# Kernel optimization log

Hardware: AMD Instinct MI355X
Metric: run time of the kernel (lower is better)

The kernel has to match this reference:

```python
import jax, jax.numpy as jnp
import numpy as np

N_NODES = 50000
N_EDGES = 800000


def sage_conv(x, src, dst, W_l, b_l, W_r, num_nodes):
    """PyG SAGEConv with mean aggregation: out = lin_l(mean_agg(neighbors)) + lin_r(x)."""
    # gather source-node features per edge, scatter-mean into destination nodes
    msg = x[src]                                                   # [E, F]
    agg = jax.ops.segment_sum(msg, dst, num_segments=num_nodes)    # [N, F]
    cnt = jax.ops.segment_sum(jnp.ones((src.shape[0],), x.dtype), dst,
                              num_segments=num_nodes)              # [N]
    agg = agg / jnp.maximum(cnt, 1.0)[:, None]
    return agg @ W_l + b_l + x @ W_r


def setup_inputs() -> dict:
    key = jax.random.key(0)
    ks = jax.random.split(key, 8)
    d_in, d_hid, d_out = 128, 256, 128
    s = lambda k, shape, fan: jax.random.normal(k, shape, jnp.float32) / np.sqrt(fan)
    return {
        "x": jax.random.normal(ks[0], (N_NODES, d_in), jnp.float32),
        "edge_index": jax.random.randint(ks[1], (2, N_EDGES), 0, N_NODES, jnp.int64),
        "W1_l": s(ks[2], (d_in, d_hid), d_in),
        "b1": jnp.zeros((d_hid,), jnp.float32),
        "W1_r": s(ks[3], (d_in, d_hid), d_in),
        "W2_l": s(ks[4], (d_hid, d_out), d_hid),
        "b2": jnp.zeros((d_out,), jnp.float32),
        "W2_r": s(ks[5], (d_hid, d_out), d_hid),
    }


def reference(x, edge_index, W1_l, b1, W1_r, W2_l, b2, W2_r):
    src, dst = edge_index[0], edge_index[1]
    n = x.shape[0]
    h = sage_conv(x, src, dst, W1_l, b1, W1_r, n)
    h = jax.nn.relu(h)  # dropout p=0.0 -> identity
    out = sage_conv(h, src, dst, W2_l, b2, W2_r, n)
    return out
```

## Files before the change

### kernel.cpp

```cpp
#include <hip/hip_runtime.h>
#include <hip/hip_bf16.h>
#include <stdint.h>

#define NN 50000
#define NE 800000
#define NB 196
#define EPB 2048
#define NBLK ((NE + EPB - 1) / EPB)
#define BCAP 8192

typedef __attribute__((ext_vector_type(8))) __bf16 bf16x8;
typedef __attribute__((ext_vector_type(4))) float f32x4;
typedef __attribute__((ext_vector_type(4))) int i32x4;

__device__ __forceinline__ float bflo(uint32_t u) { return __uint_as_float(u << 16); }
__device__ __forceinline__ float bfhi(uint32_t u) { return __uint_as_float(u & 0xffff0000u); }
__device__ __forceinline__ uint16_t f2bf(float f) {
    uint32_t u = __float_as_uint(f);
    u += 0x7fffu + ((u >> 16) & 1u);
    return (uint16_t)(u >> 16);
}
__device__ __forceinline__ float bf2f(uint16_t h) { return __uint_as_float(((uint32_t)h) << 16); }

__device__ __forceinline__ int xcd_swz(int bid, int nwg) {
    int q = nwg >> 3, r = nwg & 7;
    int xcd = bid & 7, idx = bid >> 3;
    int base = (xcd < r) ? xcd * (q + 1) : r * (q + 1) + (xcd - r) * q;
    return base + idx;
}

__device__ __forceinline__ int detect_i64(const int* ei, int* sh_cnt) {
    int t = threadIdx.x;
    if (t == 0) *sh_cnt = 0;
    __syncthreads();
    if (t < 64) atomicAdd(sh_cnt, (ei[2 * t + 1] != 0) ? 1 : 0);
    __syncthreads();
    return (*sh_cnt < 4) ? 1 : 0;
}

__device__ __forceinline__ int detect_fp32(const uint32_t* xu, int* sh_cnt) {
    int t = threadIdx.x;
    if (t == 0) *sh_cnt = 0;
    __syncthreads();
    uint32_t u = xu[t & 255];
    uint32_t lo = u & 0xffffu;
    uint32_t e = (lo >> 7) & 0xffu;
    int ok = (lo == 0u) || (e >= 96u && e <= 150u);
    if (t < 256) atomicAdd(sh_cnt, ok);
    __syncthreads();
    return (*sh_cnt < 192) ? 1 : 0;
}

__global__ __launch_bounds__(256) void scatter1(const int* __restrict__ ei,
                                                int* __restrict__ bucket_cur,
                                                uint32_t* __restrict__ staging) {
    __shared__ int hist[NB];
    __shared__ int curs[NB];
    __shared__ int shc;
    int fl = detect_i64(ei, &shc);
    int t = threadIdx.x;
    for (int i = t; i < NB; i += 256) hist[i] = 0;
    __syncthreads();
    int base = blockIdx.x * EPB;
    for (int i = 0; i < EPB; i += 256) {
        int e = base + i + t;
        if (e < NE) {
            int d = fl ? ei[2 * NE + 2 * e] : ei[NE + e];
            atomicAdd(&hist[d >> 8], 1);
        }
    }
    __syncthreads();
    for (int i = t; i < NB; i += 256)
        curs[i] = (hist[i] > 0) ? atomicAdd(&bucket_cur[i], hist[i]) : 0;
    __syncthreads();
    for (int i = 0; i < EPB; i += 256) {
        int e = base + i + t;
        if (e < NE) {
            int s, d;
            if (fl) { s = ei[2 * e]; d = ei[2 * NE + 2 * e]; }
            else    { s = ei[e];     d = ei[NE + e]; }
            int b = d >> 8;
            int p = atomicAdd(&curs[b], 1);
            staging[b * BCAP + p] = ((uint32_t)(d & 0xff) << 16) | (uint32_t)s;
        }
    }
}

#define NORMX_BLKS 6250
__global__ __launch_bounds__(256) void csr_norm(const uint32_t* __restrict__ staging,
                                                const int* __restrict__ bucket_cur,
                                                const void* __restrict__ x,
                                                const void* __restrict__ w1l, const void* __restrict__ b1,
                                                const void* __restrict__ w1r, const void* __restrict__ w2l,
                                                const void* __restrict__ b2, const void* __restrict__ w2r,
                                                int* __restrict__ row_start, int* __restrict__ deg,
                                                float* __restrict__ inv_deg, int* __restrict__ csr,
                                                uint32_t* __restrict__ xb,
                                                uint16_t* __restrict__ w1l_sw, uint16_t* __restrict__ w1r_sw,
                                                uint16_t* __restrict__ w2l_sw, uint16_t* __restrict__ w2r_sw,
                                                uint16_t* __restrict__ bias_buf) {
    int blk = blockIdx.x;
    int t = threadIdx.x;
    if (blk < NB) {
        __shared__ int degs[256];
        __shared__ int sm[256];
        __shared__ int curs[256];
        int beg = blk * BCAP, cnt = bucket_cur[blk];
        degs[t] = 0;
        __syncthreads();
        for (int i = t; i < cnt; i += 256) atomicAdd(&degs[(staging[beg + i] >> 16) & 0xff], 1);
        __syncthreads();
        int d = degs[t];
        sm[t] = d;
        __syncthreads();
        for (int o = 1; o < 256; o <<= 1) {
            int x2 = (t >= o) ? sm[t - o] : 0;
            __syncthreads();
            sm[t] += x2;
            __syncthreads();
        }
        int excl = sm[t] - d;
        curs[t] = excl;
        int node = blk * 256 + t;
        if (node < NN) {
            row_start[node] = beg + excl;
            deg[node] = d;
            inv_deg[node] = 1.0f / (float)(d > 0 ? d : 1);
        }
        __syncthreads();
        for (int i = t; i < cnt; i += 256) {
            uint32_t u = staging[beg + i];
            int dl = (u >> 16) & 0xff;
            int p = atomicAdd(&curs[dl], 1);
            csr[beg + p] = (int)(u & 0xffffu);
        }
        return;
    }
    __shared__ int shc;
    int fp32 = detect_fp32((const uint32_t*)x, &shc);
    int nb = blk - NB;
    if (nb < NORMX_BLKS) {
        int i = nb * 256 + t;
        if (fp32) {
            f32x4 v = ((const f32x4*)x)[i];
            uint2 o;
            o.x = (uint32_t)f2bf(v[0]) | ((uint32_t)f2bf(v[1]) << 16);
            o.y = (uint32_t)f2bf(v[2]) | ((uint32_t)f2bf(v[3]) << 16);
            ((uint2*)xb)[i] = o;
        } else {
            ((uint2*)xb)[i] = ((const uint2*)x)[i];
        }
        return;
    }
    int tid = (nb - NORMX_BLKS) * 256 + t;
    if (tid < 16384) {
        int frag = tid >> 6, lane = tid & 63;
        const void* srcw; uint16_t* dst; int N; int fl;
        if (frag < 64)       { srcw = w1l; dst = w1l_sw; N = 256; fl = frag; }
        else if (frag < 128) { srcw = w1r; dst = w1r_sw; N = 256; fl = frag - 64; }
        else if (frag < 192) { srcw = w2l; dst = w2l_sw; N = 128; fl = frag - 128; }
        else                 { srcw = w2r; dst = w2r_sw; N = 128; fl = frag - 192; }
        int NTm = N >> 4;
        int kt = fl / NTm, nt = fl - kt * NTm;
        int k0 = kt * 32 + (lane >> 4) * 8, n = nt * 16 + (lane & 15);
        uint16_t* d = dst + (size_t)fl * 512 + lane * 8;
#pragma unroll
        for (int j = 0; j < 8; j++) {
            int si = (k0 + j) * N + n;
            d[j] = fp32 ? f2bf(((const float*)srcw)[si]) : ((const uint16_t*)srcw)[si];
        }
    } else if (tid < 16384 + 384) {
        int j = tid - 16384;
        const void* s = (j < 256) ? b1 : b2;
        int jj = (j < 256) ? j : j - 256;
        bias_buf[j] = fp32 ? f2bf(((const float*)s)[jj]) : ((const uint16_t*)s)[jj];
    }
}

__global__ __launch_bounds__(256) void agg_mean_v2(const uint32_t* __restrict__ xu,
                                                   const int* __restrict__ row_start,
                                                   const int* __restrict__ deg,
                                                   const int* __restrict__ csr,
                                                   const float* __restrict__ inv_deg,
                                                   uint32_t* __restrict__ outu) {
    int wave = threadIdx.x >> 6, lane = threadIdx.x & 63;
    int half = lane >> 5, l = lane & 31;
    int node = blockIdx.x * 8 + wave * 2 + half;
    int beg = row_start[node], end = beg + deg[node];
    float lx[8], hx[8], ly[8], hy[8];
#pragma unroll
    for (int k = 0; k < 8; k++) { lx[k] = 0.f; hx[k] = 0.f; ly[k] = 0.f; hy[k] = 0.f; }
    int j = beg;
    for (; j + 8 <= end; j += 8) {
        int idx[8];
#pragma unroll
        for (int k = 0; k < 8; k++) idx[k] = csr[j + k];
#pragma unroll
        for (int k = 0; k < 8; k++) {
            uint2 v = *(const uint2*)(xu + (size_t)idx[k] * 64 + l * 2);
            lx[k] += bflo(v.x); hx[k] += bfhi(v.x);
            ly[k] += bflo(v.y); hy[k] += bfhi(v.y);
        }
    }
    for (; j < end; j++) {
        uint2 v = *(const uint2*)(xu + (size_t)csr[j] * 64 + l * 2);
        lx[0] += bflo(v.x); hx[0] += bfhi(v.x);
        ly[0] += bflo(v.y); hy[0] += bfhi(v.y);
    }
    float sc = inv_deg[node];
    float r0 = (((lx[0] + lx[1]) + (lx[2] + lx[3])) + ((lx[4] + lx[5]) + (lx[6] + lx[7]))) * sc;
    float r1 = (((hx[0] + hx[1]) + (hx[2] + hx[3])) + ((hx[4] + hx[5]) + (hx[6] + hx[7]))) * sc;
    float r2 = (((ly[0] + ly[1]) + (ly[2] + ly[3])) + ((ly[4] + ly[5]) + (ly[6] + ly[7]))) * sc;
    float r3 = (((hy[0] + hy[1]) + (hy[2] + hy[3])) + ((hy[4] + hy[5]) + (hy[6] + hy[7]))) * sc;
    uint2 o;
    o.x = (uint32_t)f2bf(r0) | ((uint32_t)f2bf(r1) << 16);
    o.y = (uint32_t)f2bf(r2) | ((uint32_t)f2bf(r3) << 16);
    *(uint2*)(outu + (size_t)node * 64 + l * 2) = o;
}

__global__ __launch_bounds__(256) void agg_final_v2(const uint32_t* __restrict__ tu,
                                                    const int* __restrict__ row_start,
                                                    const int* __restrict__ deg,
                                                    const int* __restrict__ csr,
                                                    const float* __restrict__ inv_deg,
                                                    const f32x4* __restrict__ u,
                                                    f32x4* __restrict__ out) {
    int wave = threadIdx.x >> 6, lane = threadIdx.x & 63;
    int half = lane >> 5, l = lane & 31;
    int node = blockIdx.x * 8 + wave * 2 + half;
    int beg = row_start[node], end = beg + deg[node];
    float lx[8], hx[8], ly[8], hy[8];
#pragma unroll
    for (int k = 0; k < 8; k++) { lx[k] = 0.f; hx[k] = 0.f; ly[k] = 0.f; hy[k] = 0.f; }
    int j = beg;
    for (; j + 8 <= end; j += 8) {
        int idx[8];
#pragma unroll
        for (int k = 0; k < 8; k++) idx[k] = csr[j + k];
#pragma unroll
        for (int k = 0; k < 8; k++) {
            uint2 v = *(const uint2*)(tu + (size_t)idx[k] * 64 + l * 2);
            lx[k] += bflo(v.x); hx[k] += bfhi(v.x);
            ly[k] += bflo(v.y); hy[k] += bfhi(v.y);
        }
    }
    for (; j < end; j++) {
        uint2 v = *(const uint2*)(tu + (size_t)csr[j] * 64 + l * 2);
        lx[0] += bflo(v.x); hx[0] += bfhi(v.x);
        ly[0] += bflo(v.y); hy[0] += bfhi(v.y);
    }
    float sc = inv_deg[node];
    f32x4 uv = u[(size_t)node * 32 + l];
    f32x4 r;
    r[0] = (((lx[0] + lx[1]) + (lx[2] + lx[3])) + ((lx[4] + lx[5]) + (lx[6] + lx[7]))) * sc + uv[0];
    r[1] = (((hx[0] + hx[1]) + (hx[2] + hx[3])) + ((hx[4] + hx[5]) + (hx[6] + hx[7]))) * sc + uv[1];
    r[2] = (((ly[0] + ly[1]) + (ly[2] + ly[3])) + ((ly[4] + ly[5]) + (ly[6] + ly[7]))) * sc + uv[2];
    r[3] = (((hy[0] + hy[1]) + (hy[2] + hy[3])) + ((hy[4] + hy[5]) + (hy[6] + hy[7]))) * sc + uv[3];
    out[(size_t)node * 32 + l] = r;
}

#define HW 264
__global__ __launch_bounds__(512) void fused_mlp(const uint16_t* __restrict__ AGG,
                                                 const uint16_t* __restrict__ XB,
                                                 const uint16_t* __restrict__ W1Lsw,
                                                 const uint16_t* __restrict__ W1Rsw,
                                                 const uint16_t* __restrict__ W2Lsw,
                                                 const uint16_t* __restrict__ W2Rsw,
                                                 const uint16_t* __restrict__ bias,
                                                 uint16_t* __restrict__ T,
                                                 float* __restrict__ U) {
    __shared__ __align__(16) uint16_t hbuf[64 * HW];
    int wg = xcd_swz(blockIdx.x, 782);
    int node0 = wg * 64;
    int tid = threadIdx.x;
    int wave = tid >> 6, lane = tid & 63;
    int wr = wave >> 2, wc = wave & 3;
    int m = lane & 15, q = lane >> 4;

    int ar[2];
#pragma unroll
    for (int rf = 0; rf < 2; rf++) {
        int r = node0 + wr * 32 + rf * 16 + m;
        ar[rf] = (r < NN) ? r : (NN - 1);
    }

    {
        f32x4 acc[2][4];
#pragma unroll
        for (int rf = 0; rf < 2; rf++)
#pragma unroll
            for (int nt = 0; nt < 4; nt++)
#pragma unroll
                for (int i = 0; i < 4; i++) acc[rf][nt][i] = 0.f;

#pragma unroll
        for (int kt = 0; kt < 4; kt++) {
            bf16x8 a10 = *(const bf16x8*)(AGG + (size_t)ar[0] * 128 + kt * 32 + q * 8);
            bf16x8 a11 = *(const bf16x8*)(AGG + (size_t)ar[1] * 128 + kt * 32 + q * 8);
            bf16x8 a20 = *(const bf16x8*)(XB + (size_t)ar[0] * 128 + kt * 32 + q * 8);
            bf16x8 a21 = *(const bf16x8*)(XB + (size_t)ar[1] * 128 + kt * 32 + q * 8);
#pragma unroll
            for (int nt = 0; nt < 4; nt++) {
                int gnt = wc * 4 + nt;
                bf16x8 B1 = *(const bf16x8*)(W1Lsw + ((size_t)(kt * 16 + gnt)) * 512 + lane * 8);
                bf16x8 B2 = *(const bf16x8*)(W1Rsw + ((size_t)(kt * 16 + gnt)) * 512 + lane * 8);
                acc[0][nt] = __builtin_amdgcn_mfma_f32_16x16x32_bf16(a10, B1, acc[0][nt], 0, 0, 0);
                acc[1][nt] = __builtin_amdgcn_mfma_f32_16x16x32_bf16(a11, B1, acc[1][nt], 0, 0, 0);
                acc[0][nt] = __builtin_amdgcn_mfma_f32_16x16x32_bf16(a20, B2, acc[0][nt], 0, 0, 0);
                acc[1][nt] = __builtin_amdgcn_mfma_f32_16x16x32_bf16(a21, B2, acc[1][nt], 0, 0, 0);
            }
        }
#pragma unroll
        for (int rf = 0; rf < 2; rf++)
#pragma unroll
            for (int nt = 0; nt < 4; nt++) {
                int cl = wc * 64 + nt * 16 + m;
                float bv = bf2f(bias[cl]);
#pragma unroll
                for (int i = 0; i < 4; i++) {
                    float v = fmaxf(acc[rf][nt][i] + bv, 0.f);
                    hbuf[(wr * 32 + rf * 16 + q * 4 + i) * HW + cl] = f2bf(v);
                }
            }
    }
    __syncthreads();

    f32x4 acc1[2][2], acc2[2][2];
#pragma unroll
    for (int rf = 0; rf < 2; rf++)
#pragma unroll
        for (int nt = 0; nt < 2; nt++)
#pragma unroll
            for (int i = 0; i < 4; i++) { acc1[rf][nt][i] = 0.f; acc2[rf][nt][i] = 0.f; }

#pragma unroll
    for (int kt = 0; kt < 8; kt++) {
        bf16x8 a0 = *(const bf16x8*)&hbuf[(wr * 32 + m) * HW + kt * 32 + q * 8];
        bf16x8 a1 = *(const bf16x8*)&hbuf[(wr * 32 + 16 + m) * HW + kt * 32 + q * 8];
#pragma unroll
        for (int nt = 0; nt < 2; nt++) {
            int gnt = wc * 2 + nt;
            bf16x8 BL = *(const bf16x8*)(W2Lsw + ((size_t)(kt * 8 + gnt)) * 512 + lane * 8);
            bf16x8 BR = *(const bf16x8*)(W2Rsw + ((size_t)(kt * 8 + gnt)) * 512 + lane * 8);
            acc1[0][nt] = __builtin_amdgcn_mfma_f32_16x16x32_bf16(a0, BL, acc1[0][nt], 0, 0, 0);
            acc1[1][nt] = __builtin_amdgcn_mfma_f32_16x16x32_bf16(a1, BL, acc1[1][nt], 0, 0, 0);
            acc2[0][nt] = __builtin_amdgcn_mfma_f32_16x16x32_bf16(a0, BR, acc2[0][nt], 0, 0, 0);
            acc2[1][nt] = __builtin_amdgcn_mfma_f32_16x16x32_bf16(a1, BR, acc2[1][nt], 0, 0, 0);
        }
    }
    __syncthreads();

    {
        uint16_t* st = hbuf;
#pragma unroll
        for (int rf = 0; rf < 2; rf++)
#pragma unroll
            for (int nt = 0; nt < 2; nt++) {
                int cl = wc * 32 + nt * 16 + m;
#pragma unroll
                for (int i = 0; i < 4; i++)
                    st[(wr * 32 + rf * 16 + q * 4 + i) * 136 + cl] = f2bf(acc1[rf][nt][i]);
            }
        __syncthreads();
#pragma unroll
        for (int rr = 0; rr < 2; rr++) {
            int row = rr * 32 + (tid >> 4);
            int grow = node0 + row;
            if (grow < NN)
                *(i32x4*)(T + (size_t)grow * 128 + (tid & 15) * 8) =
                    *(const i32x4*)&st[row * 136 + (tid & 15) * 8];
        }
        __syncthreads();
    }

    {
        float* su = (float*)hbuf;
#pragma unroll
        for (int rf = 0; rf < 2; rf++)
#pragma unroll
            for (int nt = 0; nt < 2; nt++) {
                int cl = wc * 32 + nt * 16 + m;
                float bv = bf2f(bias[256 + cl]);
#pragma unroll
                for (int i = 0; i < 4; i++)
                    su[(wr * 32 + rf * 16 + q * 4 + i) * 132 + cl] = acc2[rf][nt][i] + bv;
            }
        __syncthreads();
#pragma unroll
        for (int rr = 0; rr < 4; rr++) {
            int row = rr * 16 + (tid >> 5);
            int grow = node0 + row;
            if (grow < NN)
                *(f32x4*)(U + (size_t)grow * 128 + (tid & 31) * 4) =
                    *(const f32x4*)&su[row * 132 + (tid & 31) * 4];
        }
    }
}

extern "C" void kernel_launch(void* const* d_in, const int* in_sizes, int n_in,
                              void* d_out, int out_size, void* d_ws, size_t ws_size,
                              hipStream_t stream) {
    const void* x_raw  = d_in[0];
    const int*  ei     = (const int*)d_in[1];
    const void* W1l    = d_in[2];
    const void* b1     = d_in[3];
    const void* W1r    = d_in[4];
    const void* W2l    = d_in[5];
    const void* b2     = d_in[6];
    const void* W2r    = d_in[7];

    uint8_t* ws = (uint8_t*)d_ws;
    size_t off = 0;
    auto alloc = [&](size_t b) -> void* {
        void* p = ws + off;
        off += (b + 255) & ~(size_t)255;
        return p;
    };
    int*      bucket_cur  = (int*)alloc((NB + 4) * 4);
    int*      deg         = (int*)alloc((size_t)NN * 4);
    float*    inv_deg     = (float*)alloc((size_t)NN * 4);
    int*      row_start   = (int*)alloc((size_t)NN * 4);
    int*      csr         = (int*)alloc((size_t)NB * BCAP * 4);
    uint32_t* xb          = (uint32_t*)alloc((size_t)NN * 64 * 4);
    uint16_t* bias_buf    = (uint16_t*)alloc(384 * 2);
    uint16_t* agg         = (uint16_t*)alloc((size_t)NN * 128 * 2);
    uint16_t* t           = (uint16_t*)alloc((size_t)NN * 128 * 2);
    float*    u           = (float*)alloc((size_t)NN * 128 * 4);
    uint16_t* w1l_sw      = (uint16_t*)alloc(128 * 256 * 2);
    uint16_t* w1r_sw      = (uint16_t*)alloc(128 * 256 * 2);
    uint16_t* w2l_sw      = (uint16_t*)alloc(256 * 128 * 2);
    uint16_t* w2r_sw      = (uint16_t*)alloc(256 * 128 * 2);

    uint32_t* staging = (uint32_t*)t;

    hipMemsetAsync(bucket_cur, 0, NB * 4, stream);
    scatter1<<<NBLK, 256, 0, stream>>>(ei, bucket_cur, staging);
    csr_norm<<<NB + NORMX_BLKS + 66, 256, 0, stream>>>(staging, bucket_cur, x_raw,
                                                       W1l, b1, W1r, W2l, b2, W2r,
                                                       row_start, deg, inv_deg, csr,
                                                       xb, w1l_sw, w1r_sw, w2l_sw, w2r_sw, bias_buf);

    agg_mean_v2<<<NN / 8, 256, 0, stream>>>(xb, row_start, deg, csr, inv_deg, (uint32_t*)agg);
    fused_mlp<<<782, 512, 0, stream>>>(agg, (const uint16_t*)xb,
                                       w1l_sw, w1r_sw, w2l_sw, w2r_sw, bias_buf, t, u);
    agg_final_v2<<<NN / 8, 256, 0, stream>>>((const uint32_t*)t, row_start, deg, csr, inv_deg,
                                             (const f32x4*)u, (f32x4*)d_out);
}
```

Measured before the change: 238.1 us.

## Split final aggregation by column slice per XCD with atomic work queues

```diff
diff --git a/kernel.cpp b/kernel.cpp
--- a/kernel.cpp
+++ b/kernel.cpp
@@ -8,6 +8,7 @@
 #define EPB 2048
 #define NBLK ((NE + EPB - 1) / EPB)
 #define BCAP 8192
+#define NGRP 782
 
 typedef __attribute__((ext_vector_type(8))) __bf16 bf16x8;
 typedef __attribute__((ext_vector_type(4))) float f32x4;
@@ -218,45 +219,74 @@
     *(uint2*)(outu + (size_t)node * 64 + l * 2) = o;
 }
 
-__global__ __launch_bounds__(256) void agg_final_v2(const uint32_t* __restrict__ tu,
-                                                    const int* __restrict__ row_start,
-                                                    const int* __restrict__ deg,
-                                                    const int* __restrict__ csr,
-                                                    const float* __restrict__ inv_deg,
-                                                    const f32x4* __restrict__ u,
-                                                    f32x4* __restrict__ out) {
-    int wave = threadIdx.x >> 6, lane = threadIdx.x & 63;
-    int half = lane >> 5, l = lane & 31;
-    int node = blockIdx.x * 8 + wave * 2 + half;
-    int beg = row_start[node], end = beg + deg[node];
-    float lx[8], hx[8], ly[8], hy[8];
-#pragma unroll
-    for (int k = 0; k < 8; k++) { lx[k] = 0.f; hx[k] = 0.f; ly[k] = 0.f; hy[k] = 0.f; }
-    int j = beg;
-    for (; j + 8 <= end; j += 8) {
-        int idx[8];
-#pragma unroll
-        for (int k = 0; k < 8; k++) idx[k] = csr[j + k];
-#pragma unroll
-        for (int k = 0; k < 8; k++) {
-            uint2 v = *(const uint2*)(tu + (size_t)idx[k] * 64 + l * 2);
-            lx[k] += bflo(v.x); hx[k] += bfhi(v.x);
-            ly[k] += bflo(v.y); hy[k] += bfhi(v.y);
-        }
-    }
-    for (; j < end; j++) {
-        uint2 v = *(const uint2*)(tu + (size_t)csr[j] * 64 + l * 2);
-        lx[0] += bflo(v.x); hx[0] += bfhi(v.x);
-        ly[0] += bflo(v.y); hy[0] += bfhi(v.y);
-    }
-    float sc = inv_deg[node];
-    f32x4 uv = u[(size_t)node * 32 + l];
-    f32x4 r;
-    r[0] = (((lx[0] + lx[1]) + (lx[2] + lx[3])) + ((lx[4] + lx[5]) + (lx[6] + lx[7]))) * sc + uv[0];
-    r[1] = (((hx[0] + hx[1]) + (hx[2] + hx[3])) + ((hx[4] + hx[5]) + (hx[6] + hx[7]))) * sc + uv[1];
-    r[2] = (((ly[0] + ly[1]) + (ly[2] + ly[3])) + ((ly[4] + ly[5]) + (ly[6] + ly[7]))) * sc + uv[2];
-    r[3] = (((hy[0] + hy[1]) + (hy[2] + hy[3])) + ((hy[4] + hy[5]) + (hy[6] + hy[7]))) * sc + uv[3];
-    out[(size_t)node * 32 + l] = r;
+__global__ __launch_bounds__(256) void agg_final_q(const uint32_t* __restrict__ tu,
+                                                   const int* __restrict__ row_start,
+                                                   const int* __restrict__ deg,
+                                                   const int* __restrict__ csr,
+                                                   const float* __restrict__ inv_deg,
+                                                   const float* __restrict__ u,
+                                                   int* __restrict__ qctr,
+                                                   float* __restrict__ out) {
+    __shared__ int sh_idx;
+    int t = threadIdx.x;
+    int hw = t >> 5, l = t & 31;
+    int esub = l >> 2, dpair = l & 3;
+    uint32_t myxcd;
+    asm volatile("s_getreg_b32 %0, hwreg(HW_REG_XCC_ID)" : "=s"(myxcd));
+    myxcd &= 7u;
+    for (int ss = 0; ss < 8; ss++) {
+        int s = (int)((myxcd + ss) & 7u);
+        int colu = s * 8 + dpair * 2;
+        while (true) {
+            __syncthreads();
+            if (t == 0) sh_idx = atomicAdd(&qctr[s], 1);
+            __syncthreads();
+            int g = sh_idx;
+            if (g >= NGRP) break;
+            for (int it = 0; it < 8; it++) {
+                int node = g * 64 + hw * 8 + it;
+                if (node >= NN) break;
+                int beg = row_start[node], d = deg[node];
+                float f0 = 0.f, f1 = 0.f, f2 = 0.f, f3 = 0.f;
+                int j = 0;
+                for (; j + 16 <= d; j += 16) {
+                    int i0 = csr[beg + j + esub];
+                    int i1 = csr[beg + j + 8 + esub];
+                    uint2 v0 = *(const uint2*)(tu + (size_t)i0 * 64 + colu);
+                    uint2 v1 = *(const uint2*)(tu + (size_t)i1 * 64 + colu);
+                    f0 += bflo(v0.x) + bflo(v1.x);
+                    f1 += bfhi(v0.x) + bfhi(v1.x);
+                    f2 += bflo(v0.y) + bflo(v1.y);
+                    f3 += bfhi(v0.y) + bfhi(v1.y);
+                }
+                for (; j < d; j += 8) {
+                    if (j + esub < d) {
+                        int i0 = csr[beg + j + esub];
+                        uint2 v0 = *(const uint2*)(tu + (size_t)i0 * 64 + colu);
+                        f0 += bflo(v0.x); f1 += bfhi(v0.x);
+                        f2 += bflo(v0.y); f3 += bfhi(v0.y);
+                    }
+                }
+#pragma unroll
+                for (int mask = 4; mask <= 16; mask <<= 1) {
+                    f0 += __shfl_xor(f0, mask);
+                    f1 += __shfl_xor(f1, mask);
+                    f2 += __shfl_xor(f2, mask);
+                    f3 += __shfl_xor(f3, mask);
+                }
+                if (esub == 0) {
+                    float sc = inv_deg[node];
+                    f32x4 uv = *(const f32x4*)(u + (size_t)node * 128 + s * 16 + dpair * 4);
+                    f32x4 r;
+                    r[0] = f0 * sc + uv[0];
+                    r[1] = f1 * sc + uv[1];
+                    r[2] = f2 * sc + uv[2];
+                    r[3] = f3 * sc + uv[3];
+                    __builtin_nontemporal_store(r, (f32x4*)(out + (size_t)node * 128 + s * 16 + dpair * 4));
+                }
+            }
+        }
+    }
 }
 
 #define HW 264
@@ -416,7 +446,7 @@
         off += (b + 255) & ~(size_t)255;
         return p;
     };
-    int*      bucket_cur  = (int*)alloc((NB + 4) * 4);
+    int*      bucket_cur  = (int*)alloc((NB + 16) * 4);
     int*      deg         = (int*)alloc((size_t)NN * 4);
     float*    inv_deg     = (float*)alloc((size_t)NN * 4);
     int*      row_start   = (int*)alloc((size_t)NN * 4);
@@ -431,9 +461,11 @@
     uint16_t* w2l_sw      = (uint16_t*)alloc(256 * 128 * 2);
     uint16_t* w2r_sw      = (uint16_t*)alloc(256 * 128 * 2);
 
+    int* qctr = bucket_cur + NB + 4;
+
     uint32_t* staging = (uint32_t*)t;
 
-    hipMemsetAsync(bucket_cur, 0, NB * 4, stream);
+    hipMemsetAsync(bucket_cur, 0, (NB + 16) * 4, stream);
     scatter1<<<NBLK, 256, 0, stream>>>(ei, bucket_cur, staging);
     csr_norm<<<NB + NORMX_BLKS + 66, 256, 0, stream>>>(staging, bucket_cur, x_raw,
                                                        W1l, b1, W1r, W2l, b2, W2r,
@@ -443,6 +475,6 @@
     agg_mean_v2<<<NN / 8, 256, 0, stream>>>(xb, row_start, deg, csr, inv_deg, (uint32_t*)agg);
     fused_mlp<<<782, 512, 0, stream>>>(agg, (const uint16_t*)xb,
                                        w1l_sw, w1r_sw, w2l_sw, w2r_sw, bias_buf, t, u);
-    agg_final_v2<<<NN / 8, 256, 0, stream>>>((const uint32_t*)t, row_start, deg, csr, inv_deg,
-                                             (const f32x4*)u, (f32x4*)d_out);
-}
+    agg_final_q<<<2048, 256, 0, stream>>>((const uint32_t*)t, row_start, deg, csr, inv_deg,
+                                          u, qctr, (float*)d_out);
+}
```

After: 507.0 us. +112.9%, slower.
